# Kernel optimization log

Measured on AMD Instinct MI355X. Metric: run time of the kernel, lower is better.

## Reference

```python
import jax, jax.numpy as jnp
import numpy as np

HIDDEN = 768
VOCAB = 32000
HS1 = 128


def setup_inputs() -> dict:
    key = jax.random.key(0)
    k_tk, k_hs, k_w1, k_b1, k_w2, k_b2 = jax.random.split(key, 6)
    B, S = 16, 4096
    tk = jax.random.randint(k_tk, (B, S), 0, VOCAB, dtype=jnp.int64)
    hs0 = jax.random.normal(k_hs, (B, S, HIDDEN), dtype=jnp.float32)
    # lin1: in_features = VOCAB + HIDDEN, out = HS1.  Stored as [in, out]
    # (transpose of torch's [out, in]); rows [0:VOCAB] multiply the one-hot,
    # rows [VOCAB:] multiply hs0, matching cat([one_hot, hs0], -1).
    bound1 = 1.0 / np.sqrt(VOCAB + HIDDEN)
    W1 = jax.random.uniform(k_w1, (VOCAB + HIDDEN, HS1), jnp.float32, -bound1, bound1)
    b1 = jax.random.uniform(k_b1, (HS1,), jnp.float32, -bound1, bound1)
    bound2 = 1.0 / np.sqrt(HS1)
    W2 = jax.random.uniform(k_w2, (HS1, 1), jnp.float32, -bound2, bound2)
    b2 = jax.random.uniform(k_b2, (1,), jnp.float32, -bound2, bound2)
    return {"tk": tk, "hs0": hs0, "W1": W1, "b1": b1, "W2": W2, "b2": b2}


def reference(tk, hs0, W1, b1, W2, b2):
    # one_hot(tk) @ W1[:VOCAB] is exactly a row gather (entries are 0/1),
    # so compute it as a gather fused with the hs0 projection.
    tok_part = W1[:VOCAB][tk]                      # [B, S, HS1] gather
    hs_part = jnp.einsum("bsh,hk->bsk", hs0, W1[VOCAB:])  # [B, S, HS1]
    h = jax.nn.relu(tok_part + hs_part + b1)       # [B, S, HS1]
    out = jnp.einsum("bsk,ko->bso", h, W2) + b2    # [B, S, 1]
    return out.squeeze(-1)                         # [B, S]
```

## Files before the change

kernel.cpp:

```cpp
#include <hip/hip_runtime.h>

#define HIDDEN 768
#define VOCAB  32000
#define HS1    128
#define NSTAGE 24
#define LSTRIDE 36

typedef __attribute__((ext_vector_type(8))) short bf16x8;
typedef __attribute__((ext_vector_type(4))) float f32x4;

__device__ __forceinline__ unsigned short f2bf(float f) {
    union { float f; unsigned u; } x; x.f = f;
    unsigned r = x.u + 0x7fffu + ((x.u >> 16) & 1u);
    return (unsigned short)(r >> 16);
}

__global__ void pack_b_kernel(const float* __restrict__ W1,
                              unsigned short* __restrict__ Bp) {
    int tid = blockIdx.x * 256 + threadIdx.x;
    float v = W1[(size_t)VOCAB * HS1 + tid];
    int k = tid >> 7;
    int n = tid & 127;
    int ks = k >> 5, kr = k & 31;
    int quad = kr >> 3, j = kr & 7;
    int nt = n >> 4, c = n & 15;
    int lane = quad * 16 + c;
    Bp[(((ks * 8 + nt) * 64 + lane) << 3) + j] = f2bf(v);
}

__launch_bounds__(256, 2)
__global__ void classifier_kernel(const int* __restrict__ tk,
                                  const float* __restrict__ hs0,
                                  const float* __restrict__ W1,
                                  const float* __restrict__ b1,
                                  const float* __restrict__ W2,
                                  const float* __restrict__ b2,
                                  const unsigned short* __restrict__ Bp,
                                  float* __restrict__ out) {
    __shared__ float lds[4][2][32 * LSTRIDE];

    const int lane = threadIdx.x & 63;
    const int wave = threadIdx.x >> 6;
    const int quad = lane >> 4;
    const int col  = lane & 15;
    const int row0 = (blockIdx.x * 4 + wave) * 32;

    float* buf0 = &lds[wave][0][0];
    float* buf1 = &lds[wave][1][0];

    const int srow = lane >> 3;
    const int scol = (lane & 7) * 4;
    const float* gbase = hs0 + (size_t)row0 * HIDDEN;

    int toks[8];
#pragma unroll
    for (int mt = 0; mt < 2; ++mt)
#pragma unroll
        for (int reg = 0; reg < 4; ++reg)
            toks[mt * 4 + reg] = tk[row0 + mt * 16 + quad * 4 + reg];

    f32x4 acc[2][8];
#pragma unroll
    for (int mt = 0; mt < 2; ++mt)
#pragma unroll
        for (int nt = 0; nt < 8; ++nt)
            acc[mt][nt] = (f32x4){0.f, 0.f, 0.f, 0.f};

    f32x4 gA[4], gB[4];
    auto gload = [&](f32x4* g, int s) {
#pragma unroll
        for (int i = 0; i < 4; ++i) {
            const float* p = gbase + (size_t)(i * 8 + srow) * HIDDEN + s * 32 + scol;
            g[i] = __builtin_nontemporal_load((const f32x4*)p);
        }
    };
    auto lstore = [&](float* buf, const f32x4* g) {
#pragma unroll
        for (int i = 0; i < 4; ++i)
            *(f32x4*)(buf + (i * 8 + srow) * LSTRIDE + scol) = g[i];
    };

    const unsigned short* pb0 = Bp + lane * 8;
    auto loadB = [&](int kstep, bf16x8* b) {
        const unsigned short* pb = pb0 + kstep * 4096;
#pragma unroll
        for (int nt = 0; nt < 4; ++nt) {
            b[nt]     = *(const bf16x8*)(pb + nt * 512);
            b[nt + 4] = *(const bf16x8*)(pb + 2048 + nt * 512);
        }
    };

    auto cvt8 = [&](f32x4 lo, f32x4 hi) {
        bf16x8 r;
        r[0] = (short)f2bf(lo[0]); r[1] = (short)f2bf(lo[1]);
        r[2] = (short)f2bf(lo[2]); r[3] = (short)f2bf(lo[3]);
        r[4] = (short)f2bf(hi[0]); r[5] = (short)f2bf(hi[1]);
        r[6] = (short)f2bf(hi[2]); r[7] = (short)f2bf(hi[3]);
        return r;
    };

    auto stage_body = [&](int s, float* cur, float* alt, f32x4* gs,
                          const bf16x8* bc, bf16x8* bn) {
        if (s + 1 < NSTAGE) loadB(s + 1, bn);
        if (s + 1 < NSTAGE) lstore(alt, gs);
        if (s + 3 < NSTAGE) gload(gs, s + 3);
        const float* p0 = cur + col * LSTRIDE + quad * 8;
        const float* p1 = p0 + 16 * LSTRIDE;
        f32x4 a0l = *(const f32x4*)p0, a0h = *(const f32x4*)(p0 + 4);
        f32x4 a1l = *(const f32x4*)p1, a1h = *(const f32x4*)(p1 + 4);
        bf16x8 af0 = cvt8(a0l, a0h);
        bf16x8 af1 = cvt8(a1l, a1h);
#pragma unroll
        for (int nt = 0; nt < 8; ++nt) {
            acc[0][nt] = __builtin_amdgcn_mfma_f32_16x16x32_bf16(af0, bc[nt], acc[0][nt], 0, 0, 0);
            acc[1][nt] = __builtin_amdgcn_mfma_f32_16x16x32_bf16(af1, bc[nt], acc[1][nt], 0, 0, 0);
        }
    };

    bf16x8 bfrA[8], bfrB[8];
    gload(gA, 0);
    gload(gB, 1);
    lstore(buf0, gA);
    gload(gA, 2);
    loadB(0, bfrA);

#pragma unroll 1
    for (int s = 0; s < NSTAGE; s += 2) {
        stage_body(s,     buf0, buf1, gB, bfrA, bfrB);
        stage_body(s + 1, buf1, buf0, gA, bfrB, bfrA);
    }

    const float bb2 = b2[0];
    float b1v[8], w2v[8];
#pragma unroll
    for (int nt = 0; nt < 8; ++nt) {
        b1v[nt] = b1[nt * 16 + col];
        w2v[nt] = W2[nt * 16 + col];
    }
#pragma unroll
    for (int mt = 0; mt < 2; ++mt) {
#pragma unroll
        for (int reg = 0; reg < 4; ++reg) {
            int r = row0 + mt * 16 + quad * 4 + reg;
            const float* wrow = W1 + (size_t)toks[mt * 4 + reg] * HS1;
            float p = 0.f;
#pragma unroll
            for (int nt = 0; nt < 8; ++nt) {
                float v = acc[mt][nt][reg] + wrow[nt * 16 + col] + b1v[nt];
                v = fmaxf(v, 0.f);
                p = fmaf(v, w2v[nt], p);
            }
            p += __shfl_xor(p, 1);
            p += __shfl_xor(p, 2);
            p += __shfl_xor(p, 4);
            p += __shfl_xor(p, 8);
            if (col == 0) out[r] = p + bb2;
        }
    }
}

extern "C" void kernel_launch(void* const* d_in, const int* in_sizes, int n_in,
                              void* d_out, int out_size, void* d_ws, size_t ws_size,
                              hipStream_t stream) {
    const int*   tk  = (const int*)d_in[0];
    const float* hs0 = (const float*)d_in[1];
    const float* W1  = (const float*)d_in[2];
    const float* b1  = (const float*)d_in[3];
    const float* W2  = (const float*)d_in[4];
    const float* b2  = (const float*)d_in[5];
    float* out = (float*)d_out;
    unsigned short* Bp = (unsigned short*)d_ws;

    pack_b_kernel<<<(HIDDEN * HS1) / 256, 256, 0, stream>>>(W1, Bp);

    int n_tokens = in_sizes[0];
    int grid = n_tokens / 128;
    classifier_kernel<<<grid, 256, 0, stream>>>(tk, hs0, W1, b1, W2, b2, Bp, out);
}
```

Baseline: 292.4 us.

## Load hs0 directly into MFMA registers and prefetch token rows via LDS DMA

The hs0 A-operand is now read straight from global memory into registers in the MFMA fragment layout, removing the LDS staging round-trip. The per-row W1 token gather is issued at kernel start with global_load_lds into LDS, so it overlaps the main loop, and is waited on with an explicit vmcnt(0) before the epilogue. Direct global loads have a less coalesced pattern (each lane reads 32 bytes per row) and only two stages of prefetch, which may expose more memory latency.

```diff
diff --git a/kernel.cpp b/kernel.cpp
--- a/kernel.cpp
+++ b/kernel.cpp
@@ -4,7 +4,6 @@
 #define VOCAB  32000
 #define HS1    128
 #define NSTAGE 24
-#define LSTRIDE 36
 
 typedef __attribute__((ext_vector_type(8))) short bf16x8;
 typedef __attribute__((ext_vector_type(4))) float f32x4;
@@ -37,7 +36,7 @@
                                   const float* __restrict__ b2,
                                   const unsigned short* __restrict__ Bp,
                                   float* __restrict__ out) {
-    __shared__ float lds[4][2][32 * LSTRIDE];
+    __shared__ float w1c[4][32][HS1];
 
     const int lane = threadIdx.x & 63;
     const int wave = threadIdx.x >> 6;
@@ -45,19 +44,13 @@
     const int col  = lane & 15;
     const int row0 = (blockIdx.x * 4 + wave) * 32;
 
-    float* buf0 = &lds[wave][0][0];
-    float* buf1 = &lds[wave][1][0];
-
-    const int srow = lane >> 3;
-    const int scol = (lane & 7) * 4;
-    const float* gbase = hs0 + (size_t)row0 * HIDDEN;
-
-    int toks[8];
+    float b1v[8], w2v[8];
 #pragma unroll
-    for (int mt = 0; mt < 2; ++mt)
-#pragma unroll
-        for (int reg = 0; reg < 4; ++reg)
-            toks[mt * 4 + reg] = tk[row0 + mt * 16 + quad * 4 + reg];
+    for (int nt = 0; nt < 8; ++nt) {
+        b1v[nt] = b1[nt * 16 + col];
+        w2v[nt] = W2[nt * 16 + col];
+    }
+    const int mytok = tk[row0 + (lane & 31)];
 
     f32x4 acc[2][8];
 #pragma unroll
@@ -66,18 +59,16 @@
         for (int nt = 0; nt < 8; ++nt)
             acc[mt][nt] = (f32x4){0.f, 0.f, 0.f, 0.f};
 
+    const float* aP0 = hs0 + (size_t)(row0 + col) * HIDDEN + quad * 8;
+    const float* aP1 = aP0 + (size_t)16 * HIDDEN;
     f32x4 gA[4], gB[4];
-    auto gload = [&](f32x4* g, int s) {
-#pragma unroll
-        for (int i = 0; i < 4; ++i) {
-            const float* p = gbase + (size_t)(i * 8 + srow) * HIDDEN + s * 32 + scol;
-            g[i] = __builtin_nontemporal_load((const f32x4*)p);
-        }
-    };
-    auto lstore = [&](float* buf, const f32x4* g) {
-#pragma unroll
-        for (int i = 0; i < 4; ++i)
-            *(f32x4*)(buf + (i * 8 + srow) * LSTRIDE + scol) = g[i];
+    auto loadA = [&](f32x4* a, int s) {
+        const float* p0 = aP0 + s * 32;
+        const float* p1 = aP1 + s * 32;
+        a[0] = __builtin_nontemporal_load((const f32x4*)p0);
+        a[1] = __builtin_nontemporal_load((const f32x4*)(p0 + 4));
+        a[2] = __builtin_nontemporal_load((const f32x4*)p1);
+        a[3] = __builtin_nontemporal_load((const f32x4*)(p1 + 4));
     };
 
     const unsigned short* pb0 = Bp + lane * 8;
@@ -99,17 +90,29 @@
         return r;
     };
 
-    auto stage_body = [&](int s, float* cur, float* alt, f32x4* gs,
-                          const bf16x8* bc, bf16x8* bn) {
+    bf16x8 bfrA[8], bfrB[8];
+    loadA(gA, 0);
+    loadA(gB, 1);
+    loadB(0, bfrA);
+
+    {
+        float* dst0 = &w1c[wave][0][0];
+#pragma unroll
+        for (int p = 0; p < 16; ++p) {
+            int t = __shfl(mytok, 2 * p + (lane >> 5));
+            const float* src = W1 + (size_t)t * HS1 + (lane & 31) * 4;
+            __builtin_amdgcn_global_load_lds(
+                (const __attribute__((address_space(1))) void*)src,
+                (__attribute__((address_space(3))) void*)(dst0 + p * 2 * HS1),
+                16, 0, 0);
+        }
+    }
+
+    auto stage_body = [&](int s, f32x4* a, const bf16x8* bc, bf16x8* bn) {
         if (s + 1 < NSTAGE) loadB(s + 1, bn);
-        if (s + 1 < NSTAGE) lstore(alt, gs);
-        if (s + 3 < NSTAGE) gload(gs, s + 3);
-        const float* p0 = cur + col * LSTRIDE + quad * 8;
-        const float* p1 = p0 + 16 * LSTRIDE;
-        f32x4 a0l = *(const f32x4*)p0, a0h = *(const f32x4*)(p0 + 4);
-        f32x4 a1l = *(const f32x4*)p1, a1h = *(const f32x4*)(p1 + 4);
-        bf16x8 af0 = cvt8(a0l, a0h);
-        bf16x8 af1 = cvt8(a1l, a1h);
+        bf16x8 af0 = cvt8(a[0], a[1]);
+        bf16x8 af1 = cvt8(a[2], a[3]);
+        if (s + 2 < NSTAGE) loadA(a, s + 2);
 #pragma unroll
         for (int nt = 0; nt < 8; ++nt) {
             acc[0][nt] = __builtin_amdgcn_mfma_f32_16x16x32_bf16(af0, bc[nt], acc[0][nt], 0, 0, 0);
@@ -117,36 +120,25 @@
         }
     };
 
-    bf16x8 bfrA[8], bfrB[8];
-    gload(gA, 0);
-    gload(gB, 1);
-    lstore(buf0, gA);
-    gload(gA, 2);
-    loadB(0, bfrA);
-
 #pragma unroll 1
     for (int s = 0; s < NSTAGE; s += 2) {
-        stage_body(s,     buf0, buf1, gB, bfrA, bfrB);
-        stage_body(s + 1, buf1, buf0, gA, bfrB, bfrA);
+        stage_body(s,     gA, bfrA, bfrB);
+        stage_body(s + 1, gB, bfrB, bfrA);
     }
 
+    asm volatile("s_waitcnt vmcnt(0)" ::: "memory");
+
     const float bb2 = b2[0];
-    float b1v[8], w2v[8];
-#pragma unroll
-    for (int nt = 0; nt < 8; ++nt) {
-        b1v[nt] = b1[nt * 16 + col];
-        w2v[nt] = W2[nt * 16 + col];
-    }
 #pragma unroll
     for (int mt = 0; mt < 2; ++mt) {
 #pragma unroll
         for (int reg = 0; reg < 4; ++reg) {
-            int r = row0 + mt * 16 + quad * 4 + reg;
-            const float* wrow = W1 + (size_t)toks[mt * 4 + reg] * HS1;
+            int lr = mt * 16 + quad * 4 + reg;
+            const float* wl = &w1c[wave][lr][0];
             float p = 0.f;
 #pragma unroll
             for (int nt = 0; nt < 8; ++nt) {
-                float v = acc[mt][nt][reg] + wrow[nt * 16 + col] + b1v[nt];
+                float v = acc[mt][nt][reg] + wl[nt * 16 + col] + b1v[nt];
                 v = fmaxf(v, 0.f);
                 p = fmaf(v, w2v[nt], p);
             }
@@ -154,7 +146,7 @@
             p += __shfl_xor(p, 2);
             p += __shfl_xor(p, 4);
             p += __shfl_xor(p, 8);
-            if (col == 0) out[r] = p + bb2;
+            if (col == 0) out[row0 + lr] = p + bb2;
         }
     }
 }
```

New measurement: 307.3 us. +5.1%, slower.
